# Performance work log

Measured on AMD Instinct MI355X. Metric: run time of the kernel, lower is better.

## Reference

```python
import jax, jax.numpy as jnp
import numpy as np

EMBED = 1024
HEADS = 16


def setup_inputs() -> dict:
    key = jax.random.key(0)
    ks = jax.random.split(key, 7)
    scale = 1.0 / np.sqrt(EMBED)
    x = jax.random.normal(ks[0], (4, 2048, EMBED), dtype=jnp.float32)
    Wq = jax.random.normal(ks[1], (EMBED, EMBED), dtype=jnp.float32) * scale
    bq = jax.random.normal(ks[2], (EMBED,), dtype=jnp.float32) * 0.01
    Wk = jax.random.normal(ks[3], (EMBED, EMBED), dtype=jnp.float32) * scale
    bk = jax.random.normal(ks[4], (EMBED,), dtype=jnp.float32) * 0.01
    Wv = jax.random.normal(ks[5], (EMBED, EMBED), dtype=jnp.float32) * scale
    bv = jax.random.normal(ks[6], (EMBED,), dtype=jnp.float32) * 0.01
    return {"x": x, "Wq": Wq, "bq": bq, "Wk": Wk, "bk": bk, "Wv": Wv, "bv": bv}


def reference(x, Wq, bq, Wk, bk, Wv, bv):
    b, s, n = x.shape
    h = HEADS
    d = n // h
    # torch nn.Linear: y = x @ W.T + b
    q = (jnp.einsum("bsn,mn->bsm", x, Wq) + bq).reshape(b, s, h, d).transpose(0, 2, 1, 3)
    k = (jnp.einsum("bsn,mn->bsm", x, Wk) + bk).reshape(b, s, h, d).transpose(0, 2, 1, 3)
    v = (jnp.einsum("bsn,mn->bsm", x, Wv) + bv).reshape(b, s, h, d).transpose(0, 2, 1, 3)
    # scores: [b, h, s_q, s_k]; fixed scale of 1/10 as in the source
    scores = jnp.einsum("bhqd,bhkd->bhqk", q, k) / 10.0
    # NOTE: softmax over dim=-2 (the QUERY axis), matching the source exactly
    attn = jax.nn.softmax(scores, axis=-2)
    out = jnp.einsum("bhqk,bhkd->bhqd", attn, v)
    return out.transpose(0, 2, 1, 3).reshape(b, s, n)
```

## Files before the change

### kernel.cpp

```cpp
#include <hip/hip_runtime.h>
#include <math.h>

#define SEQ    2048
#define EMBED  1024
#define HEADS  16
#define HDIM   64
#define BATCH  4
#define ROWS   (BATCH * SEQ)
#define BH     (BATCH * HEADS)

typedef _Float16 f16;
typedef __attribute__((ext_vector_type(8))) _Float16 f16x8;
typedef __attribute__((ext_vector_type(4))) _Float16 f16x4;
typedef __attribute__((ext_vector_type(4))) float    f32x4;

#define LOG2E_10 0.14426950408889634f

__device__ __forceinline__ float fast_exp2(float x) { return __builtin_amdgcn_exp2f(x); }
__device__ __forceinline__ float fast_log2(float x) { return __builtin_amdgcn_logf(x); }

__device__ __forceinline__ void async16(void* l, const void* g) {
    __builtin_amdgcn_global_load_lds(
        (__attribute__((address_space(1))) void*)(uintptr_t)g,
        (__attribute__((address_space(3))) void*)(uint32_t)(uintptr_t)l,
        16, 0, 0);
}
__device__ __forceinline__ void async4(void* l, const void* g) {
    __builtin_amdgcn_global_load_lds(
        (__attribute__((address_space(1))) void*)(uintptr_t)g,
        (__attribute__((address_space(3))) void*)(uint32_t)(uintptr_t)l,
        4, 0, 0);
}

__device__ __forceinline__ f32x4 mfma16(f16x8 a, f16x8 b, f32x4 c) {
    return __builtin_amdgcn_mfma_f32_16x16x32_f16(a, b, c, 0, 0, 0);
}

#define NX4 (ROWS * EMBED / 4)
#define NW4 (EMBED * EMBED / 4)
__global__ __launch_bounds__(256) void cvt_kernel(
    const float* __restrict__ x,
    const float* __restrict__ Wq, const float* __restrict__ Wk,
    const float* __restrict__ Wv,
    f16* __restrict__ xh, f16* __restrict__ Wh)
{
    int i = blockIdx.x * 256 + threadIdx.x;
    const float4* src; f16* dst; int j;
    if (i < NX4)              { src = (const float4*)x;  dst = xh;                j = i; }
    else if (i < NX4 + NW4)   { src = (const float4*)Wq; dst = Wh;                j = i - NX4; }
    else if (i < NX4 + 2*NW4) { src = (const float4*)Wk; dst = Wh + EMBED*EMBED;  j = i - NX4 - NW4; }
    else                      { src = (const float4*)Wv; dst = Wh + 2*EMBED*EMBED;j = i - NX4 - 2*NW4; }
    float4 v = src[j];
    f16x4 h;
    h[0] = (f16)v.x; h[1] = (f16)v.y; h[2] = (f16)v.z; h[3] = (f16)v.w;
    *(f16x4*)(dst + (size_t)j * 4) = h;
}

__global__ __launch_bounds__(256) void proj_kernel(
    const f16* __restrict__ A,
    const f16* __restrict__ W,
    const float* __restrict__ bq, const float* __restrict__ bk,
    const float* __restrict__ bv,
    f16* __restrict__ Qh, f16* __restrict__ Kh, f16* __restrict__ Vt)
{
    __shared__ f16 As[128 * 32];
    __shared__ f16 Bs[128 * 32];

    const int t = threadIdx.x, wv = t >> 6, lane = t & 63;
    const int lm = lane & 15, quad = lane >> 4;
    const int r0 = blockIdx.x * 128, c0 = blockIdx.y * 128;
    const int wm = wv & 1, wn = wv >> 1;

    const int srow = wv * 32 + (lane >> 2);
    const int sch  = (lane & 3) * 8;
    const f16* gA = A + (size_t)(r0 + srow) * EMBED + sch;
    const f16* gB = W + (size_t)(c0 + srow) * EMBED + sch;
    f16* lA = As + wv * 1024;
    f16* lB = Bs + wv * 1024;

    f32x4 acc[4][4];
#pragma unroll
    for (int i = 0; i < 4; ++i)
#pragma unroll
        for (int j = 0; j < 4; ++j) acc[i][j] = (f32x4){0.f, 0.f, 0.f, 0.f};

    for (int kk = 0; kk < EMBED; kk += 32) {
        __syncthreads();
        async16(lA,        gA + kk);
        async16(lA + 512,  gA + 16 * EMBED + kk);
        async16(lB,        gB + kk);
        async16(lB + 512,  gB + 16 * EMBED + kk);
        __syncthreads();

        f16x8 af[4], bf[4];
#pragma unroll
        for (int i = 0; i < 4; ++i)
            af[i] = *(const f16x8*)&As[(wm * 64 + i * 16 + lm) * 32 + quad * 8];
#pragma unroll
        for (int i = 0; i < 4; ++i)
            bf[i] = *(const f16x8*)&Bs[(wn * 64 + i * 16 + lm) * 32 + quad * 8];
#pragma unroll
        for (int mi = 0; mi < 4; ++mi)
#pragma unroll
            for (int ni = 0; ni < 4; ++ni)
                acc[mi][ni] = mfma16(af[mi], bf[ni], acc[mi][ni]);
    }

    const int z = c0 >> 10;
    const float* bias = (z == 0) ? bq : (z == 1) ? bk : bv;
#pragma unroll
    for (int ni = 0; ni < 4; ++ni) {
        int col = c0 + wn * 64 + ni * 16 + lm;
        int cz  = col & 1023;
        float bb = bias[cz];
        int h = cz >> 6, d = cz & 63;
#pragma unroll
        for (int mi = 0; mi < 4; ++mi) {
            int rbase = r0 + wm * 64 + mi * 16 + quad * 4;
            int b = rbase >> 11, s = rbase & 2047;
            if (z < 2) {
                f16* O = (z == 0) ? Qh : Kh;
                size_t base = ((size_t)(b * HEADS + h) * SEQ + s) * HDIM + d;
#pragma unroll
                for (int r = 0; r < 4; ++r)
                    O[base + (size_t)r * HDIM] = (f16)(acc[mi][ni][r] + bb);
            } else {
                f16x4 pk;
#pragma unroll
                for (int r = 0; r < 4; ++r) pk[r] = (f16)(acc[mi][ni][r] + bb);
                *(f16x4*)&Vt[((size_t)(b * HEADS + h) * HDIM + d) * SEQ + s] = pk;
            }
        }
    }
}

__global__ __launch_bounds__(256) void stats_kernel(
    const f16* __restrict__ Qh, const f16* __restrict__ Kh,
    float* __restrict__ lgv)
{
    __shared__ f16 Ks[128 * 64];
    __shared__ f16 Qs[64 * 64];

    const int t = threadIdx.x, wv = t >> 6, lane = t & 63;
    const int lm = lane & 15, quad = lane >> 4;
    const int bh = blockIdx.y, k0 = blockIdx.x * 128;
    const int grow = lane >> 3;
    const int gsw  = ((lane & 7) ^ grow) * 8;
    const int rs   = lm & 7;
    const size_t base = (size_t)bh * SEQ * HDIM;

#pragma unroll
    for (int i = 0; i < 4; ++i) {
        int g = wv * 4 + i;
        async16(Ks + g * 512, Kh + base + (size_t)(k0 + g * 8 + grow) * HDIM + gsw);
    }
    __syncthreads();

    f16x8 kf[2][2];
#pragma unroll
    for (int ct = 0; ct < 2; ++ct)
#pragma unroll
        for (int ds = 0; ds < 2; ++ds)
            kf[ct][ds] = *(const f16x8*)&Ks[(wv * 32 + ct * 16 + lm) * 64
                                            + (((ds * 4 + quad) ^ rs) << 3)];

    float cs0 = 0.f, cs1 = 0.f;
    for (int q0 = 0; q0 < SEQ; q0 += 64) {
        __syncthreads();
#pragma unroll
        for (int i = 0; i < 2; ++i) {
            int g = wv * 2 + i;
            async16(Qs + g * 512, Qh + base + (size_t)(q0 + g * 8 + grow) * HDIM + gsw);
        }
        __syncthreads();
#pragma unroll
        for (int qt = 0; qt < 4; ++qt) {
            f16x8 a0 = *(const f16x8*)&Qs[(qt * 16 + lm) * 64 + ((quad ^ rs) << 3)];
            f16x8 a1 = *(const f16x8*)&Qs[(qt * 16 + lm) * 64 + (((4 + quad) ^ rs) << 3)];
            f32x4 c0v = (f32x4){0.f, 0.f, 0.f, 0.f};
            f32x4 c1v = (f32x4){0.f, 0.f, 0.f, 0.f};
            c0v = mfma16(a0, kf[0][0], c0v); c0v = mfma16(a1, kf[0][1], c0v);
            c1v = mfma16(a0, kf[1][0], c1v); c1v = mfma16(a1, kf[1][1], c1v);
#pragma unroll
            for (int r = 0; r < 4; ++r) {
                cs0 += fast_exp2(c0v[r] * LOG2E_10);
                cs1 += fast_exp2(c1v[r] * LOG2E_10);
            }
        }
    }
    cs0 += __shfl_xor(cs0, 16, 64); cs0 += __shfl_xor(cs0, 32, 64);
    cs1 += __shfl_xor(cs1, 16, 64); cs1 += __shfl_xor(cs1, 32, 64);
    if (quad == 0) {
        lgv[(size_t)bh * SEQ + k0 + wv * 32 + lm]      = 10.0f - fast_log2(cs0);
        lgv[(size_t)bh * SEQ + k0 + wv * 32 + 16 + lm] = 10.0f - fast_log2(cs1);
    }
}

__global__ __launch_bounds__(256) void out_kernel(
    const f16* __restrict__ Qh, const f16* __restrict__ Kh,
    const f16* __restrict__ Vt, const float* __restrict__ lgv,
    float* __restrict__ out)
{
    __shared__ f16 Ps[4 * 32 * 72];
    __shared__ f16 Ks[64 * 64];
    __shared__ f16 Vs[64 * 64];
    __shared__ float Ls[64];

    const int t = threadIdx.x, wv = t >> 6, lane = t & 63;
    const int lm = lane & 15, quad = lane >> 4;
    const int bh = blockIdx.y, q0 = blockIdx.x * 128;
    const int b = bh >> 4, h = bh & 15;
    const int grow = lane >> 3;
    const int gsw  = ((lane & 7) ^ grow) * 8;
    const int rs   = lm & 7;
    const size_t base = (size_t)bh * SEQ * HDIM;

#pragma unroll
    for (int i = 0; i < 4; ++i) {
        int g = wv * 4 + i;
        async16(Ps + g * 512, Qh + base + (size_t)(q0 + g * 8 + grow) * HDIM + gsw);
    }
    __syncthreads();
    f16x8 qa[2][2];
#pragma unroll
    for (int qs = 0; qs < 2; ++qs)
#pragma unroll
        for (int ds = 0; ds < 2; ++ds)
            qa[qs][ds] = *(const f16x8*)&Ps[(wv * 32 + qs * 16 + lm) * 64
                                            + (((ds * 4 + quad) ^ rs) << 3)];

    f32x4 oacc[2][4];
#pragma unroll
    for (int i = 0; i < 2; ++i)
#pragma unroll
        for (int j = 0; j < 4; ++j) oacc[i][j] = (f32x4){0.f, 0.f, 0.f, 0.f};

    f16* Pw = Ps + wv * (32 * 72);

    for (int k0 = 0; k0 < SEQ; k0 += 64) {
        __syncthreads();
#pragma unroll
        for (int i = 0; i < 2; ++i) {
            int g = wv * 2 + i;
            async16(Ks + g * 512, Kh + base + (size_t)(k0 + g * 8 + grow) * HDIM + gsw);
            async16(Vs + g * 512, Vt + base + (size_t)(g * 8 + grow) * SEQ + k0 + gsw);
        }
        if (wv == 0) async4(Ls, lgv + (size_t)bh * SEQ + k0 + lane);
        __syncthreads();

#pragma unroll
        for (int ct = 0; ct < 4; ++ct) {
            int krow = ct * 16 + lm;
            f16x8 kf0 = *(const f16x8*)&Ks[krow * 64 + ((quad ^ rs) << 3)];
            f16x8 kf1 = *(const f16x8*)&Ks[krow * 64 + (((4 + quad) ^ rs) << 3)];
            float lg[4];
#pragma unroll
            for (int r = 0; r < 4; ++r) lg[r] = Ls[ct * 16 + quad * 4 + r];
#pragma unroll
            for (int qs = 0; qs < 2; ++qs) {
                f32x4 s4 = (f32x4){0.f, 0.f, 0.f, 0.f};
                s4 = mfma16(kf0, qa[qs][0], s4);
                s4 = mfma16(kf1, qa[qs][1], s4);
                f16x4 pk;
#pragma unroll
                for (int r = 0; r < 4; ++r)
                    pk[r] = (f16)fast_exp2(s4[r] * LOG2E_10 + lg[r]);
                *(f16x4*)&Pw[(qs * 16 + lm) * 72 + ct * 16 + quad * 4] = pk;
            }
        }
#pragma unroll
        for (int ks = 0; ks < 2; ++ks) {
            f16x8 pa0 = *(const f16x8*)&Pw[(lm) * 72 + ks * 32 + quad * 8];
            f16x8 pa1 = *(const f16x8*)&Pw[(16 + lm) * 72 + ks * 32 + quad * 8];
#pragma unroll
            for (int dt = 0; dt < 4; ++dt) {
                f16x8 vb = *(const f16x8*)&Vs[(dt * 16 + lm) * 64
                                              + (((ks * 4 + quad) ^ rs) << 3)];
                oacc[0][dt] = mfma16(pa0, vb, oacc[0][dt]);
                oacc[1][dt] = mfma16(pa1, vb, oacc[1][dt]);
            }
        }
    }

    const float inv1024 = 1.0f / 1024.0f;
#pragma unroll
    for (int qt = 0; qt < 2; ++qt)
#pragma unroll
        for (int dt = 0; dt < 4; ++dt) {
            int col = h * HDIM + dt * 16 + lm;
#pragma unroll
            for (int r = 0; r < 4; ++r) {
                int s = q0 + wv * 32 + qt * 16 + quad * 4 + r;
                out[((size_t)b * SEQ + s) * EMBED + col] = oacc[qt][dt][r] * inv1024;
            }
        }
}

extern "C" void kernel_launch(void* const* d_in, const int* in_sizes, int n_in,
                              void* d_out, int out_size, void* d_ws, size_t ws_size,
                              hipStream_t stream) {
    const float* x  = (const float*)d_in[0];
    const float* Wq = (const float*)d_in[1];
    const float* bq = (const float*)d_in[2];
    const float* Wk = (const float*)d_in[3];
    const float* bk = (const float*)d_in[4];
    const float* Wv = (const float*)d_in[5];
    const float* bv = (const float*)d_in[6];
    float* out = (float*)d_out;

    f16* xh = (f16*)d_ws;
    f16* Wh = xh + (size_t)ROWS * EMBED;
    f16* Qh = Wh + (size_t)3 * EMBED * EMBED;
    f16* Kh = Qh + (size_t)BH * SEQ * HDIM;
    f16* Vt = Kh + (size_t)BH * SEQ * HDIM;
    float* lgv = (float*)(Vt + (size_t)BH * SEQ * HDIM);

    cvt_kernel<<<(NX4 + 3 * NW4) / 256, 256, 0, stream>>>(x, Wq, Wk, Wv, xh, Wh);
    proj_kernel<<<dim3(ROWS / 128, 3 * EMBED / 128), 256, 0, stream>>>(
        xh, Wh, bq, bk, bv, Qh, Kh, Vt);
    stats_kernel<<<dim3(SEQ / 128, BH), 256, 0, stream>>>(Qh, Kh, lgv);
    out_kernel<<<dim3(SEQ / 128, BH), 256, 0, stream>>>(Qh, Kh, Vt, lgv, out);
}
```

Before: 308.7 us.

## Double-buffer LDS tiles and remap attention blocks across XCDs

The projection GEMM, the column-stats kernel and the output kernel now use two LDS buffers. The next K/Q/V tile is prefetched with async global-to-LDS loads while the current tile is computed, which leaves one barrier per iteration instead of two. The stats and output kernels switch to a 1-D grid whose index is decoded so that consecutive blocks on the same XCD share a batch-head and reuse its K/V in that XCD's L2. The cost is double the LDS for these buffers, which may lower occupancy, plus an extra barrier in the output kernel before Q staging is reused for P.

```diff
diff --git a/kernel.cpp b/kernel.cpp
--- a/kernel.cpp
+++ b/kernel.cpp
@@ -63,8 +63,8 @@
     const float* __restrict__ bv,
     f16* __restrict__ Qh, f16* __restrict__ Kh, f16* __restrict__ Vt)
 {
-    __shared__ f16 As[128 * 32];
-    __shared__ f16 Bs[128 * 32];
+    __shared__ f16 As[2][128 * 32];
+    __shared__ f16 Bs[2][128 * 32];
 
     const int t = threadIdx.x, wv = t >> 6, lane = t & 63;
     const int lm = lane & 15, quad = lane >> 4;
@@ -75,8 +75,7 @@
     const int sch  = (lane & 3) * 8;
     const f16* gA = A + (size_t)(r0 + srow) * EMBED + sch;
     const f16* gB = W + (size_t)(c0 + srow) * EMBED + sch;
-    f16* lA = As + wv * 1024;
-    f16* lB = Bs + wv * 1024;
+    const int lofs = wv * 1024;
 
     f32x4 acc[4][4];
 #pragma unroll
@@ -84,26 +83,34 @@
 #pragma unroll
         for (int j = 0; j < 4; ++j) acc[i][j] = (f32x4){0.f, 0.f, 0.f, 0.f};
 
-    for (int kk = 0; kk < EMBED; kk += 32) {
-        __syncthreads();
-        async16(lA,        gA + kk);
-        async16(lA + 512,  gA + 16 * EMBED + kk);
-        async16(lB,        gB + kk);
-        async16(lB + 512,  gB + 16 * EMBED + kk);
-        __syncthreads();
-
+    async16(&As[0][lofs],       gA);
+    async16(&As[0][lofs + 512], gA + 16 * EMBED);
+    async16(&Bs[0][lofs],       gB);
+    async16(&Bs[0][lofs + 512], gB + 16 * EMBED);
+    __syncthreads();
+
+    for (int it = 0; it < EMBED / 32; ++it) {
+        const int cur = it & 1, nxt = cur ^ 1;
+        if (it + 1 < EMBED / 32) {
+            const int kk = (it + 1) * 32;
+            async16(&As[nxt][lofs],       gA + kk);
+            async16(&As[nxt][lofs + 512], gA + 16 * EMBED + kk);
+            async16(&Bs[nxt][lofs],       gB + kk);
+            async16(&Bs[nxt][lofs + 512], gB + 16 * EMBED + kk);
+        }
         f16x8 af[4], bf[4];
 #pragma unroll
         for (int i = 0; i < 4; ++i)
-            af[i] = *(const f16x8*)&As[(wm * 64 + i * 16 + lm) * 32 + quad * 8];
+            af[i] = *(const f16x8*)&As[cur][(wm * 64 + i * 16 + lm) * 32 + quad * 8];
 #pragma unroll
         for (int i = 0; i < 4; ++i)
-            bf[i] = *(const f16x8*)&Bs[(wn * 64 + i * 16 + lm) * 32 + quad * 8];
+            bf[i] = *(const f16x8*)&Bs[cur][(wn * 64 + i * 16 + lm) * 32 + quad * 8];
 #pragma unroll
         for (int mi = 0; mi < 4; ++mi)
 #pragma unroll
             for (int ni = 0; ni < 4; ++ni)
                 acc[mi][ni] = mfma16(af[mi], bf[ni], acc[mi][ni]);
+        __syncthreads();
     }
 
     const int z = c0 >> 10;
@@ -134,16 +141,24 @@
     }
 }
 
+__device__ __forceinline__ void xcd_decode(int d, int& bh, int& x128) {
+    int xcd  = d & 7;
+    int r    = d >> 3;
+    x128     = (r & 15) * 128;
+    bh       = (r >> 4) * 8 + xcd;
+}
+
 __global__ __launch_bounds__(256) void stats_kernel(
     const f16* __restrict__ Qh, const f16* __restrict__ Kh,
     float* __restrict__ lgv)
 {
     __shared__ f16 Ks[128 * 64];
-    __shared__ f16 Qs[64 * 64];
+    __shared__ f16 Qs[2][64 * 64];
 
     const int t = threadIdx.x, wv = t >> 6, lane = t & 63;
     const int lm = lane & 15, quad = lane >> 4;
-    const int bh = blockIdx.y, k0 = blockIdx.x * 128;
+    int bh, k0;
+    xcd_decode(blockIdx.x, bh, k0);
     const int grow = lane >> 3;
     const int gsw  = ((lane & 7) ^ grow) * 8;
     const int rs   = lm & 7;
@@ -154,6 +169,11 @@
         int g = wv * 4 + i;
         async16(Ks + g * 512, Kh + base + (size_t)(k0 + g * 8 + grow) * HDIM + gsw);
     }
+#pragma unroll
+    for (int i = 0; i < 2; ++i) {
+        int g = wv * 2 + i;
+        async16(&Qs[0][g * 512], Qh + base + (size_t)(g * 8 + grow) * HDIM + gsw);
+    }
     __syncthreads();
 
     f16x8 kf[2][2];
@@ -165,18 +185,21 @@
                                             + (((ds * 4 + quad) ^ rs) << 3)];
 
     float cs0 = 0.f, cs1 = 0.f;
-    for (int q0 = 0; q0 < SEQ; q0 += 64) {
-        __syncthreads();
-#pragma unroll
-        for (int i = 0; i < 2; ++i) {
-            int g = wv * 2 + i;
-            async16(Qs + g * 512, Qh + base + (size_t)(q0 + g * 8 + grow) * HDIM + gsw);
-        }
-        __syncthreads();
+    for (int it = 0; it < SEQ / 64; ++it) {
+        const int cur = it & 1, nxt = cur ^ 1;
+        if (it + 1 < SEQ / 64) {
+            const int q0 = (it + 1) * 64;
+#pragma unroll
+            for (int i = 0; i < 2; ++i) {
+                int g = wv * 2 + i;
+                async16(&Qs[nxt][g * 512],
+                        Qh + base + (size_t)(q0 + g * 8 + grow) * HDIM + gsw);
+            }
+        }
 #pragma unroll
         for (int qt = 0; qt < 4; ++qt) {
-            f16x8 a0 = *(const f16x8*)&Qs[(qt * 16 + lm) * 64 + ((quad ^ rs) << 3)];
-            f16x8 a1 = *(const f16x8*)&Qs[(qt * 16 + lm) * 64 + (((4 + quad) ^ rs) << 3)];
+            f16x8 a0 = *(const f16x8*)&Qs[cur][(qt * 16 + lm) * 64 + ((quad ^ rs) << 3)];
+            f16x8 a1 = *(const f16x8*)&Qs[cur][(qt * 16 + lm) * 64 + (((4 + quad) ^ rs) << 3)];
             f32x4 c0v = (f32x4){0.f, 0.f, 0.f, 0.f};
             f32x4 c1v = (f32x4){0.f, 0.f, 0.f, 0.f};
             c0v = mfma16(a0, kf[0][0], c0v); c0v = mfma16(a1, kf[0][1], c0v);
@@ -187,6 +210,7 @@
                 cs1 += fast_exp2(c1v[r] * LOG2E_10);
             }
         }
+        __syncthreads();
     }
     cs0 += __shfl_xor(cs0, 16, 64); cs0 += __shfl_xor(cs0, 32, 64);
     cs1 += __shfl_xor(cs1, 16, 64); cs1 += __shfl_xor(cs1, 32, 64);
@@ -202,13 +226,14 @@
     float* __restrict__ out)
 {
     __shared__ f16 Ps[4 * 32 * 72];
-    __shared__ f16 Ks[64 * 64];
-    __shared__ f16 Vs[64 * 64];
-    __shared__ float Ls[64];
+    __shared__ f16 Ks[2][64 * 64];
+    __shared__ f16 Vs[2][64 * 64];
+    __shared__ float Ls[2][64];
 
     const int t = threadIdx.x, wv = t >> 6, lane = t & 63;
     const int lm = lane & 15, quad = lane >> 4;
-    const int bh = blockIdx.y, q0 = blockIdx.x * 128;
+    int bh, q0;
+    xcd_decode(blockIdx.x, bh, q0);
     const int b = bh >> 4, h = bh & 15;
     const int grow = lane >> 3;
     const int gsw  = ((lane & 7) ^ grow) * 8;
@@ -220,7 +245,15 @@
         int g = wv * 4 + i;
         async16(Ps + g * 512, Qh + base + (size_t)(q0 + g * 8 + grow) * HDIM + gsw);
     }
+#pragma unroll
+    for (int i = 0; i < 2; ++i) {
+        int g = wv * 2 + i;
+        async16(&Ks[0][g * 512], Kh + base + (size_t)(g * 8 + grow) * HDIM + gsw);
+        async16(&Vs[0][g * 512], Vt + base + (size_t)(g * 8 + grow) * SEQ + gsw);
+    }
+    if (wv == 0) async4(&Ls[0][0], lgv + (size_t)bh * SEQ + lane);
     __syncthreads();
+
     f16x8 qa[2][2];
 #pragma unroll
     for (int qs = 0; qs < 2; ++qs)
@@ -228,6 +261,7 @@
         for (int ds = 0; ds < 2; ++ds)
             qa[qs][ds] = *(const f16x8*)&Ps[(wv * 32 + qs * 16 + lm) * 64
                                             + (((ds * 4 + quad) ^ rs) << 3)];
+    __syncthreads();
 
     f32x4 oacc[2][4];
 #pragma unroll
@@ -237,25 +271,29 @@
 
     f16* Pw = Ps + wv * (32 * 72);
 
-    for (int k0 = 0; k0 < SEQ; k0 += 64) {
-        __syncthreads();
-#pragma unroll
-        for (int i = 0; i < 2; ++i) {
-            int g = wv * 2 + i;
-            async16(Ks + g * 512, Kh + base + (size_t)(k0 + g * 8 + grow) * HDIM + gsw);
-            async16(Vs + g * 512, Vt + base + (size_t)(g * 8 + grow) * SEQ + k0 + gsw);
-        }
-        if (wv == 0) async4(Ls, lgv + (size_t)bh * SEQ + k0 + lane);
-        __syncthreads();
+    for (int it = 0; it < SEQ / 64; ++it) {
+        const int cur = it & 1, nxt = cur ^ 1;
+        if (it + 1 < SEQ / 64) {
+            const int k0n = (it + 1) * 64;
+#pragma unroll
+            for (int i = 0; i < 2; ++i) {
+                int g = wv * 2 + i;
+                async16(&Ks[nxt][g * 512],
+                        Kh + base + (size_t)(k0n + g * 8 + grow) * HDIM + gsw);
+                async16(&Vs[nxt][g * 512],
+                        Vt + base + (size_t)(g * 8 + grow) * SEQ + k0n + gsw);
+            }
+            if (wv == 0) async4(&Ls[nxt][0], lgv + (size_t)bh * SEQ + k0n + lane);
+        }
 
 #pragma unroll
         for (int ct = 0; ct < 4; ++ct) {
             int krow = ct * 16 + lm;
-            f16x8 kf0 = *(const f16x8*)&Ks[krow * 64 + ((quad ^ rs) << 3)];
-            f16x8 kf1 = *(const f16x8*)&Ks[krow * 64 + (((4 + quad) ^ rs) << 3)];
-            float lg[4];
-#pragma unroll
-            for (int r = 0; r < 4; ++r) lg[r] = Ls[ct * 16 + quad * 4 + r];
+            f16x8 kf0 = *(const f16x8*)&Ks[cur][krow * 64 + ((quad ^ rs) << 3)];
+            f16x8 kf1 = *(const f16x8*)&Ks[cur][krow * 64 + (((4 + quad) ^ rs) << 3)];
+            float lgr[4];
+#pragma unroll
+            for (int r = 0; r < 4; ++r) lgr[r] = Ls[cur][ct * 16 + quad * 4 + r];
 #pragma unroll
             for (int qs = 0; qs < 2; ++qs) {
                 f32x4 s4 = (f32x4){0.f, 0.f, 0.f, 0.f};
@@ -264,7 +302,7 @@
                 f16x4 pk;
 #pragma unroll
                 for (int r = 0; r < 4; ++r)
-                    pk[r] = (f16)fast_exp2(s4[r] * LOG2E_10 + lg[r]);
+                    pk[r] = (f16)fast_exp2(s4[r] * LOG2E_10 + lgr[r]);
                 *(f16x4*)&Pw[(qs * 16 + lm) * 72 + ct * 16 + quad * 4] = pk;
             }
         }
@@ -274,12 +312,13 @@
             f16x8 pa1 = *(const f16x8*)&Pw[(16 + lm) * 72 + ks * 32 + quad * 8];
 #pragma unroll
             for (int dt = 0; dt < 4; ++dt) {
-                f16x8 vb = *(const f16x8*)&Vs[(dt * 16 + lm) * 64
-                                              + (((ks * 4 + quad) ^ rs) << 3)];
+                f16x8 vb = *(const f16x8*)&Vs[cur][(dt * 16 + lm) * 64
+                                                   + (((ks * 4 + quad) ^ rs) << 3)];
                 oacc[0][dt] = mfma16(pa0, vb, oacc[0][dt]);
                 oacc[1][dt] = mfma16(pa1, vb, oacc[1][dt]);
             }
         }
+        __syncthreads();
     }
 
     const float inv1024 = 1.0f / 1024.0f;
@@ -318,6 +357,6 @@
     cvt_kernel<<<(NX4 + 3 * NW4) / 256, 256, 0, stream>>>(x, Wq, Wk, Wv, xh, Wh);
     proj_kernel<<<dim3(ROWS / 128, 3 * EMBED / 128), 256, 0, stream>>>(
         xh, Wh, bq, bk, bv, Qh, Kh, Vt);
-    stats_kernel<<<dim3(SEQ / 128, BH), 256, 0, stream>>>(Qh, Kh, lgv);
-    out_kernel<<<dim3(SEQ / 128, BH), 256, 0, stream>>>(Qh, Kh, Vt, lgv, out);
-}
+    stats_kernel<<<dim3(SEQ / 128 * BH), 256, 0, stream>>>(Qh, Kh, lgv);
+    out_kernel<<<dim3(SEQ / 128 * BH), 256, 0, stream>>>(Qh, Kh, Vt, lgv, out);
+}
```

Result: slower. 326.3 us (+5.7%).

## Restructure out_kernel with register-resident P, double-buffered K/V, and XCD-aware block mapping

Applied to the files above, without the earlier changes.

The attention output kernel now keeps exp'd scores in registers and feeds them straight into a 16x16x16 MFMA, so the round trip of P through LDS is gone. Each wave handles 64 queries over half of each 64-key tile, with a final LDS reduction across the two key halves. K/V/lgv tiles are double-buffered, so prefetch overlaps compute and one barrier per iteration is dropped. Both attention kernels use a 1D grid decoded so that blocks of the same head land on the same XCD for L2 locality. The cost is higher register pressure (64 accumulators) and an extra reduction pass at the end.

```diff
diff --git a/kernel.cpp b/kernel.cpp
--- a/kernel.cpp
+++ b/kernel.cpp
@@ -34,6 +34,9 @@
 
 __device__ __forceinline__ f32x4 mfma16(f16x8 a, f16x8 b, f32x4 c) {
     return __builtin_amdgcn_mfma_f32_16x16x32_f16(a, b, c, 0, 0, 0);
+}
+__device__ __forceinline__ f32x4 mfma16k16(f16x4 a, f16x4 b, f32x4 c) {
+    return __builtin_amdgcn_mfma_f32_16x16x16f16(a, b, c, 0, 0, 0);
 }
 
 #define NX4 (ROWS * EMBED / 4)
@@ -134,6 +137,13 @@
     }
 }
 
+__device__ __forceinline__ void xcd_decode(int d, int& bh, int& x128) {
+    int xcd  = d & 7;
+    int r    = d >> 3;
+    x128     = (r & 15) * 128;
+    bh       = (r >> 4) * 8 + xcd;
+}
+
 __global__ __launch_bounds__(256) void stats_kernel(
     const f16* __restrict__ Qh, const f16* __restrict__ Kh,
     float* __restrict__ lgv)
@@ -143,7 +153,8 @@
 
     const int t = threadIdx.x, wv = t >> 6, lane = t & 63;
     const int lm = lane & 15, quad = lane >> 4;
-    const int bh = blockIdx.y, k0 = blockIdx.x * 128;
+    int bh, k0;
+    xcd_decode(blockIdx.x, bh, k0);
     const int grow = lane >> 3;
     const int gsw  = ((lane & 7) ^ grow) * 8;
     const int rs   = lm & 7;
@@ -201,99 +212,125 @@
     const f16* __restrict__ Vt, const float* __restrict__ lgv,
     float* __restrict__ out)
 {
-    __shared__ f16 Ps[4 * 32 * 72];
-    __shared__ f16 Ks[64 * 64];
-    __shared__ f16 Vs[64 * 64];
-    __shared__ float Ls[64];
+    __shared__ f16 L[24576 + 512];
 
     const int t = threadIdx.x, wv = t >> 6, lane = t & 63;
     const int lm = lane & 15, quad = lane >> 4;
-    const int bh = blockIdx.y, q0 = blockIdx.x * 128;
+    const int wq = wv >> 1, wk = wv & 1;
+    int bh, q0;
+    xcd_decode(blockIdx.x, bh, q0);
     const int b = bh >> 4, h = bh & 15;
     const int grow = lane >> 3;
     const int gsw  = ((lane & 7) ^ grow) * 8;
     const int rs   = lm & 7;
     const size_t base = (size_t)bh * SEQ * HDIM;
 
+    f16* Qs = L;
+
 #pragma unroll
     for (int i = 0; i < 4; ++i) {
         int g = wv * 4 + i;
-        async16(Ps + g * 512, Qh + base + (size_t)(q0 + g * 8 + grow) * HDIM + gsw);
-    }
+        async16(Qs + g * 512, Qh + base + (size_t)(q0 + g * 8 + grow) * HDIM + gsw);
+    }
+#pragma unroll
+    for (int i = 0; i < 2; ++i) {
+        int g = wv * 2 + i;
+        async16(L + 8192  + g * 512, Kh + base + (size_t)(g * 8 + grow) * HDIM + gsw);
+        async16(L + 16384 + g * 512, Vt + base + (size_t)(g * 8 + grow) * SEQ + gsw);
+    }
+    if (wv == 0) async4((float*)(L + 24576), lgv + (size_t)bh * SEQ + lane);
     __syncthreads();
-    f16x8 qa[2][2];
-#pragma unroll
-    for (int qs = 0; qs < 2; ++qs)
+
+    f16x8 qa[4][2];
+#pragma unroll
+    for (int qt = 0; qt < 4; ++qt)
 #pragma unroll
         for (int ds = 0; ds < 2; ++ds)
-            qa[qs][ds] = *(const f16x8*)&Ps[(wv * 32 + qs * 16 + lm) * 64
+            qa[qt][ds] = *(const f16x8*)&Qs[(wq * 64 + qt * 16 + lm) * 64
                                             + (((ds * 4 + quad) ^ rs) << 3)];
 
-    f32x4 oacc[2][4];
-#pragma unroll
-    for (int i = 0; i < 2; ++i)
+    f32x4 oacc[4][4];
+#pragma unroll
+    for (int i = 0; i < 4; ++i)
 #pragma unroll
         for (int j = 0; j < 4; ++j) oacc[i][j] = (f32x4){0.f, 0.f, 0.f, 0.f};
 
-    f16* Pw = Ps + wv * (32 * 72);
-
-    for (int k0 = 0; k0 < SEQ; k0 += 64) {
-        __syncthreads();
-#pragma unroll
-        for (int i = 0; i < 2; ++i) {
-            int g = wv * 2 + i;
-            async16(Ks + g * 512, Kh + base + (size_t)(k0 + g * 8 + grow) * HDIM + gsw);
-            async16(Vs + g * 512, Vt + base + (size_t)(g * 8 + grow) * SEQ + k0 + gsw);
-        }
-        if (wv == 0) async4(Ls, lgv + (size_t)bh * SEQ + k0 + lane);
-        __syncthreads();
-
-#pragma unroll
-        for (int ct = 0; ct < 4; ++ct) {
-            int krow = ct * 16 + lm;
-            f16x8 kf0 = *(const f16x8*)&Ks[krow * 64 + ((quad ^ rs) << 3)];
-            f16x8 kf1 = *(const f16x8*)&Ks[krow * 64 + (((4 + quad) ^ rs) << 3)];
-            float lg[4];
-#pragma unroll
-            for (int r = 0; r < 4; ++r) lg[r] = Ls[ct * 16 + quad * 4 + r];
-#pragma unroll
-            for (int qs = 0; qs < 2; ++qs) {
+    for (int it = 0; it < SEQ / 64; ++it) {
+        const int cur = it & 1;
+        if (it + 1 < SEQ / 64) {
+            const int nxt = cur ^ 1, k0n = (it + 1) * 64;
+            f16* Kb = L + 8192  + nxt * 4096;
+            f16* Vb = L + 16384 + nxt * 4096;
+#pragma unroll
+            for (int i = 0; i < 2; ++i) {
+                int g = wv * 2 + i;
+                async16(Kb + g * 512, Kh + base + (size_t)(k0n + g * 8 + grow) * HDIM + gsw);
+                async16(Vb + g * 512, Vt + base + (size_t)(g * 8 + grow) * SEQ + k0n + gsw);
+            }
+            if (wv == 0) async4((float*)(L + 24576) + nxt * 64,
+                                lgv + (size_t)bh * SEQ + k0n + lane);
+        }
+        const f16* Kb = L + 8192  + cur * 4096;
+        const f16* Vb = L + 16384 + cur * 4096;
+        const float* Lb = (const float*)(L + 24576) + cur * 64;
+
+#pragma unroll
+        for (int ct = 0; ct < 2; ++ct) {
+            const int kb = wk * 32 + ct * 16;
+            f16x8 kf0 = *(const f16x8*)&Kb[(kb + lm) * 64 + ((quad ^ rs) << 3)];
+            f16x8 kf1 = *(const f16x8*)&Kb[(kb + lm) * 64 + (((4 + quad) ^ rs) << 3)];
+            f32x4 lg4 = *(const f32x4*)&Lb[kb + quad * 4];
+            const int vch = ((wk * 4 + ct * 2 + (quad >> 1)) ^ rs);
+            f16x4 vb[4];
+#pragma unroll
+            for (int dt = 0; dt < 4; ++dt)
+                vb[dt] = *(const f16x4*)&Vb[(dt * 16 + lm) * 64 + vch * 8 + (quad & 1) * 4];
+#pragma unroll
+            for (int qt = 0; qt < 4; ++qt) {
                 f32x4 s4 = (f32x4){0.f, 0.f, 0.f, 0.f};
-                s4 = mfma16(kf0, qa[qs][0], s4);
-                s4 = mfma16(kf1, qa[qs][1], s4);
-                f16x4 pk;
+                s4 = mfma16(kf0, qa[qt][0], s4);
+                s4 = mfma16(kf1, qa[qt][1], s4);
+                f16x4 pa;
 #pragma unroll
                 for (int r = 0; r < 4; ++r)
-                    pk[r] = (f16)fast_exp2(s4[r] * LOG2E_10 + lg[r]);
-                *(f16x4*)&Pw[(qs * 16 + lm) * 72 + ct * 16 + quad * 4] = pk;
-            }
-        }
-#pragma unroll
-        for (int ks = 0; ks < 2; ++ks) {
-            f16x8 pa0 = *(const f16x8*)&Pw[(lm) * 72 + ks * 32 + quad * 8];
-            f16x8 pa1 = *(const f16x8*)&Pw[(16 + lm) * 72 + ks * 32 + quad * 8];
+                    pa[r] = (f16)fast_exp2(s4[r] * LOG2E_10 + lg4[r]);
+#pragma unroll
+                for (int dt = 0; dt < 4; ++dt)
+                    oacc[qt][dt] = mfma16k16(pa, vb[dt], oacc[qt][dt]);
+            }
+        }
+        __syncthreads();
+    }
+
+    float* red = (float*)L;
+    if (wk == 1) {
+#pragma unroll
+        for (int qt = 0; qt < 4; ++qt)
+#pragma unroll
+            for (int dt = 0; dt < 4; ++dt)
+#pragma unroll
+                for (int r = 0; r < 4; ++r)
+                    red[wq * 4096 + (qt * 16 + quad * 4 + r) * 64 + dt * 16 + lm]
+                        = oacc[qt][dt][r];
+    }
+    __syncthreads();
+    if (wk == 0) {
+        const float inv1024 = 1.0f / 1024.0f;
+#pragma unroll
+        for (int qt = 0; qt < 4; ++qt)
 #pragma unroll
             for (int dt = 0; dt < 4; ++dt) {
-                f16x8 vb = *(const f16x8*)&Vs[(dt * 16 + lm) * 64
-                                              + (((ks * 4 + quad) ^ rs) << 3)];
-                oacc[0][dt] = mfma16(pa0, vb, oacc[0][dt]);
-                oacc[1][dt] = mfma16(pa1, vb, oacc[1][dt]);
-            }
-        }
-    }
-
-    const float inv1024 = 1.0f / 1024.0f;
-#pragma unroll
-    for (int qt = 0; qt < 2; ++qt)
-#pragma unroll
-        for (int dt = 0; dt < 4; ++dt) {
-            int col = h * HDIM + dt * 16 + lm;
-#pragma unroll
-            for (int r = 0; r < 4; ++r) {
-                int s = q0 + wv * 32 + qt * 16 + quad * 4 + r;
-                out[((size_t)b * SEQ + s) * EMBED + col] = oacc[qt][dt][r] * inv1024;
-            }
-        }
+                int col = h * HDIM + dt * 16 + lm;
+#pragma unroll
+                for (int r = 0; r < 4; ++r) {
+                    int ql = qt * 16 + quad * 4 + r;
+                    int s  = q0 + wq * 64 + ql;
+                    float v = oacc[qt][dt][r]
+                            + red[wq * 4096 + ql * 64 + dt * 16 + lm];
+                    out[((size_t)b * SEQ + s) * EMBED + col] = v * inv1024;
+                }
+            }
+    }
 }
 
 extern "C" void kernel_launch(void* const* d_in, const int* in_sizes, int n_in,
@@ -318,6 +355,6 @@
     cvt_kernel<<<(NX4 + 3 * NW4) / 256, 256, 0, stream>>>(x, Wq, Wk, Wv, xh, Wh);
     proj_kernel<<<dim3(ROWS / 128, 3 * EMBED / 128), 256, 0, stream>>>(
         xh, Wh, bq, bk, bv, Qh, Kh, Vt);
-    stats_kernel<<<dim3(SEQ / 128, BH), 256, 0, stream>>>(Qh, Kh, lgv);
-    out_kernel<<<dim3(SEQ / 128, BH), 256, 0, stream>>>(Qh, Kh, Vt, lgv, out);
-}
+    stats_kernel<<<dim3(SEQ / 128 * BH), 256, 0, stream>>>(Qh, Kh, lgv);
+    out_kernel<<<dim3(SEQ / 128 * BH), 256, 0, stream>>>(Qh, Kh, Vt, lgv, out);
+}
```

Result: faster. 300.8 us (-2.6%).
